# Performance work log

Measured on AMD Instinct MI355X. Metric: run time of the kernel, lower is better.

The kernel has to match this reference:

```python
import jax, jax.numpy as jnp
from jax import lax
import numpy as np

SMOOTH = 1e-4
BN_EPS = 1e-5


def setup_inputs() -> dict:
    key = jax.random.key(0)
    k0, k1, k2, k3 = jax.random.split(key, 4)
    B, C, H, W = 8, 256, 32, 32
    heads, head_dim = 8, 64
    inner = heads * head_dim
    x = jax.random.normal(k0, (B, C, H, W), jnp.float32)
    w_qkv = jax.random.normal(k1, (3 * inner, C, 3, 3), jnp.float32) * 0.02
    head_scale = jax.random.normal(k2, (heads,), jnp.float32)
    w_out = jax.random.normal(k3, (C, inner, 1, 1), jnp.float32) * 0.05
    gamma = jnp.ones((C,), jnp.float32)
    beta = jnp.zeros((C,), jnp.float32)
    return {"x": x, "w_qkv": w_qkv, "head_scale": head_scale,
            "w_out": w_out, "gamma": gamma, "beta": beta}


def _relative_pos_dis(H, W):
    yy, xx = jnp.meshgrid(jnp.arange(H), jnp.arange(W), indexing="ij")
    y = yy.reshape(-1).astype(jnp.float32)
    x = xx.reshape(-1).astype(jnp.float32)
    dy = (y[:, None] - y[None, :]) / H
    dx = (x[:, None] - x[None, :]) / W
    return dy * dy + dx * dx  # [HW, HW]


def reference(x, w_qkv, head_scale, w_out, gamma, beta):
    B, C, H, W = x.shape
    heads = head_scale.shape[0]
    N = H * W
    # qkv 3x3 conv, no bias
    qkv = lax.conv_general_dilated(x, w_qkv, (1, 1), "SAME",
                                   dimension_numbers=("NCHW", "OIHW", "NCHW"))
    inner = qkv.shape[1] // 3
    d = inner // heads
    q, k, v = jnp.split(qkv, 3, axis=1)
    # 'b (g d) h w -> b g (h w) d'
    def resh(t):
        return t.reshape(B, heads, d, N).transpose(0, 1, 3, 2)
    q, k, v = resh(q), resh(k), resh(v)
    # cosine-similarity attention (smoothed)
    attn = jnp.einsum("bgnd,bgmd->bgnm", q, k)
    qn = jnp.sqrt(jnp.sum(q * q, axis=-1) + SMOOTH)  # [B,g,N]
    kn = jnp.sqrt(jnp.sum(k * k, axis=-1) + SMOOTH)
    attn = attn / (qn[:, :, :, None] * kn[:, :, None, :] + SMOOTH)
    # learned per-head Gaussian positional bias
    s = jax.nn.sigmoid(head_scale) * (0.4 - 0.003) + 0.003
    scale_factor = 1.0 / (2.0 * s * s)  # [g]
    dis = _relative_pos_dis(H, W)  # [N,N]
    pb = jnp.exp(-scale_factor[:, None, None] * dis[None, :, :])
    pb = pb / jnp.sum(pb, axis=-1, keepdims=True)
    attn = attn * pb[None]
    out = jnp.einsum("bgnm,bgmd->bgnd", attn, v)
    # 'b g (h w) d -> b (g d) h w'
    out = out.transpose(0, 1, 3, 2).reshape(B, inner, H, W)
    # output projection: 1x1 conv + BatchNorm2d (train-mode batch stats) + ReLU
    out = lax.conv_general_dilated(out, w_out, (1, 1), "VALID",
                                   dimension_numbers=("NCHW", "OIHW", "NCHW"))
    mean = jnp.mean(out, axis=(0, 2, 3))
    var = jnp.mean((out - mean[None, :, None, None]) ** 2, axis=(0, 2, 3))
    out = (out - mean[None, :, None, None]) * (
        gamma[None, :, None, None] * lax.rsqrt(var + BN_EPS)[None, :, None, None]
    ) + beta[None, :, None, None]
    return jax.nn.relu(out)
```

## Files before the change

kernel.cpp:

```cpp
#include <hip/hip_runtime.h>
#include <math.h>

#define SMOOTH 1e-4f
#define BN_EPS 1e-5f

constexpr int Bn = 8;
constexpr int Cc = 256;
constexpr int Nn = 1024;
constexpr int G = 8;
constexpr int INNER = 512;
constexpr int OC = 1536;
constexpr int KK = 2304;

typedef unsigned short u16;
typedef __bf16 bf16x8 __attribute__((ext_vector_type(8)));
typedef float f32x4 __attribute__((ext_vector_type(4)));
typedef unsigned short us8 __attribute__((ext_vector_type(8)));
typedef unsigned short us4 __attribute__((ext_vector_type(4)));

__device__ __forceinline__ u16 f2bf(float f) {
  unsigned int u = __float_as_uint(f);
  unsigned int r = (u + 0x7fffu + ((u >> 16) & 1u)) >> 16;
  return (u16)r;
}
__device__ __forceinline__ float bf2f(u16 u) {
  return __uint_as_float(((unsigned int)u) << 16);
}

__device__ __forceinline__ float waveSum(float v) {
#pragma unroll
  for (int off = 32; off > 0; off >>= 1) v += __shfl_xor(v, off, 64);
  return v;
}

__device__ __forceinline__ void gl16(const u16* g, u16* l) {
  __builtin_amdgcn_global_load_lds(
      (const __attribute__((address_space(1))) unsigned int*)g,
      (__attribute__((address_space(3))) unsigned int*)l, 16, 0, 0);
}

__device__ __forceinline__ bf16x8 ld8(const u16* p) {
  return __builtin_bit_cast(bf16x8, *reinterpret_cast<const us8*>(p));
}

__device__ __forceinline__ void barrier_raw() {
  asm volatile("" ::: "memory");
  __builtin_amdgcn_s_barrier();
  asm volatile("" ::: "memory");
  __builtin_amdgcn_sched_barrier(0);
}

__device__ __forceinline__ bf16x8 ldfrag(const u16* base, int row, int col) {
  int idx = (row * 64 + col) ^ ((row & 7) << 3);
  return ld8(base + idx);
}

__global__ __launch_bounds__(256) void prep_kernel(
    const float* __restrict__ wq, const float* __restrict__ wout,
    const float* __restrict__ x, const float* __restrict__ head_scale,
    u16* __restrict__ wA, u16* __restrict__ wB, u16* __restrict__ B2,
    float* __restrict__ etab, float* __restrict__ idn) {
  __shared__ __align__(16) char smraw[13824];
  const int bid = blockIdx.x;
  const int tid = threadIdx.x;

  if (bid < 1536) {
    float* sw = (float*)smraw;
    const int oc = bid;
    for (int i = tid; i < KK; i += 256) sw[i] = wq[(size_t)oc * KK + i];
    __syncthreads();
#pragma unroll
    for (int j = 0; j < 2; ++j) {
      int c8 = tid + j * 256;
      if (c8 < KK / 8) {
        us8 v;
#pragma unroll
        for (int e = 0; e < 8; ++e) {
          int k = c8 * 8 + e;
          int tap = k >> 8, ic = k & 255;
          v[e] = f2bf(sw[ic * 9 + tap]);
        }
        *reinterpret_cast<us8*>(wA + (size_t)oc * KK + c8 * 8) = v;
      }
    }
  } else if (bid < 1600) {
    const int idx = (bid - 1536) * 256 + tid;
    const float4 a = reinterpret_cast<const float4*>(wout)[idx * 2];
    const float4 b = reinterpret_cast<const float4*>(wout)[idx * 2 + 1];
    us8 v;
    v[0] = f2bf(a.x); v[1] = f2bf(a.y); v[2] = f2bf(a.z); v[3] = f2bf(a.w);
    v[4] = f2bf(b.x); v[5] = f2bf(b.y); v[6] = f2bf(b.z); v[7] = f2bf(b.w);
    reinterpret_cast<us8*>(wB)[idx] = v;
  } else if (bid < 2624) {
    u16* sxt = (u16*)smraw;
    const int lb = bid - 1600;
    const int b = lb >> 7;
    const int y = (lb >> 2) & 31;
    const int icc = lb & 3;
    const int ic0 = icc * 64;
    const float* xb = x + (size_t)b * Cc * Nn;
    {
      const int px = tid & 31;
      const int ic_off = tid >> 5;
#pragma unroll
      for (int r = 0; r < 3; ++r) {
        const int row = y - 1 + r;
        const bool rv = (row >= 0) && (row < 32);
#pragma unroll
        for (int pass = 0; pass < 8; ++pass) {
          const int ic2 = pass * 8 + ic_off;
          float v = rv ? xb[(size_t)(ic0 + ic2) * Nn + row * 32 + px] : 0.f;
          sxt[(r * 32 + px) * 72 + ic2] = f2bf(v);
        }
      }
    }
    __syncthreads();
    const int c8 = tid & 7;
    const int opx = tid >> 3;
    u16* dst = B2 + ((size_t)b * 1024 + y * 32 + opx) * KK + ic0 + c8 * 8;
    const us8 zero = {0, 0, 0, 0, 0, 0, 0, 0};
#pragma unroll
    for (int tap = 0; tap < 9; ++tap) {
      const int dy = tap / 3 - 1, dx = tap % 3 - 1;
      const int sxx = opx + dx;
      const bool cv = (sxx >= 0) && (sxx < 32);
      const int spos = (dy + 1) * 32 + sxx;
      us8 val = cv ? *reinterpret_cast<const us8*>(sxt + spos * 72 + c8 * 8) : zero;
      *reinterpret_cast<us8*>(dst + tap * 256) = val;
    }
  } else {
    float* et = (float*)smraw;
    float* rsum = (float*)smraw + 64;
    const int g = bid - 2624;
    const float hs = head_scale[g];
    const float sg = 1.f / (1.f + __expf(-hs));
    const float s = sg * (0.4f - 0.003f) + 0.003f;
    const float sf = 1.f / (2.f * s * s);
    if (tid < 64) {
      float v = 0.f;
      if (tid < 63) {
        float d = (float)(tid - 31) * (1.f / 32.f);
        v = __expf(-sf * d * d);
      }
      et[tid] = v;
      etab[g * 64 + tid] = v;
    }
    __syncthreads();
    if (tid < 32) {
      float sum = 0.f;
#pragma unroll
      for (int ym = 0; ym < 32; ++ym) sum += et[tid - ym + 31];
      rsum[tid] = sum;
    }
    __syncthreads();
    for (int i = tid; i < 1024; i += 256)
      idn[g * 1024 + i] = 1.f / (rsum[i >> 5] * rsum[i & 31]);
  }
}

__global__ __launch_bounds__(512, 1) void qkv_gemm_kernel(
    const u16* __restrict__ wA, const u16* __restrict__ B2,
    const float* __restrict__ idn,
    u16* __restrict__ qt, u16* __restrict__ ktp, u16* __restrict__ vt) {
  const int tid = threadIdx.x;
  const int lane = tid & 63;
  const int wv = tid >> 6;
  const int wm = wv >> 2, wn = wv & 3;
  const int h = lane >> 4, l15 = lane & 15;
  const int wgid = ((int)blockIdx.x & 7) * 32 + ((int)blockIdx.x >> 3);
  const int bm = wgid & 7;
  const int bn = wgid >> 3;
  const int m0 = bm * 192, n0 = bn * 256;

  __shared__ __align__(16) u16 smem[57344];

  const int arow = tid >> 3;
  const int aslot = (tid & 7) ^ (arow & 7);
  const u16* gA0 = wA + (size_t)(m0 + arow) * KK + aslot * 8;
  const int brow = tid >> 2;
  const int bslot = (tid & 3) ^ (((tid >> 2) & 3) ^ ((tid >> 4) & 3));
  const u16* gB0 = B2 + (size_t)(n0 + brow) * KK + bslot * 8;

  const int aX = l15 & 7;
  const int bX = (l15 & 3) ^ ((l15 >> 2) & 3);
  const u16* aBase = smem + (wm * 96 + l15) * 64;
  const u16* bBase = smem + 12288 + (wn * 64 + l15) * 32;
  const int slA0 = (h ^ aX) * 8;
  const int slA1 = ((4 + h) ^ aX) * 8;
  const int slB = (h ^ bX) * 8;

  f32x4 acc[6][4];
#pragma unroll
  for (int i = 0; i < 6; ++i)
#pragma unroll
    for (int j = 0; j < 4; ++j) acc[i][j] = (f32x4){0.f, 0.f, 0.f, 0.f};

  auto STAGE_A = [&](int pass, int dbuf, int kti) {
    gl16(gA0 + (size_t)pass * 64 * KK + kti * 64,
         smem + dbuf + pass * 4096 + tid * 8);
  };
  auto STAGE_B = [&](int kap, int pass, int dbuf, int kti) {
    gl16(gB0 + (size_t)pass * 128 * KK + kti * 64 + kap * 32,
         smem + dbuf + 12288 + kap * 8192 + pass * 4096 + tid * 8);
  };

  STAGE_A(0, 0, 0); STAGE_A(1, 0, 0); STAGE_A(2, 0, 0);
  STAGE_B(0, 0, 0, 0); STAGE_B(0, 1, 0, 0);
  STAGE_B(1, 0, 0, 0); STAGE_B(1, 1, 0, 0);
  asm volatile("s_waitcnt vmcnt(2)" ::: "memory");
  barrier_raw();

  bf16x8 af[3], bf[4];
#pragma unroll 1
  for (int kt = 0; kt < 36; ++kt) {
    const int buf = (kt & 1) * 28672;
    const int nbuf = 28672 - buf;
    const bool more = (kt < 35);

#pragma unroll
    for (int ni = 0; ni < 4; ++ni) bf[ni] = ld8(bBase + buf + ni * 512 + slB);
#pragma unroll
    for (int q = 0; q < 3; ++q) af[q] = ld8(aBase + buf + q * 1024 + slA0);
    if (more) { STAGE_A(0, nbuf, kt + 1); STAGE_A(1, nbuf, kt + 1); }
    barrier_raw();
    __builtin_amdgcn_s_setprio(1);
#pragma unroll
    for (int q = 0; q < 3; ++q)
#pragma unroll
      for (int ni = 0; ni < 4; ++ni)
        acc[q][ni] = __builtin_amdgcn_mfma_f32_16x16x32_bf16(af[q], bf[ni], acc[q][ni], 0, 0, 0);
    __builtin_amdgcn_s_setprio(0);

#pragma unroll
    for (int q = 0; q < 3; ++q) af[q] = ld8(aBase + buf + (3 + q) * 1024 + slA0);
    if (more) {
      STAGE_A(2, nbuf, kt + 1); STAGE_B(0, 0, nbuf, kt + 1);
      asm volatile("s_waitcnt vmcnt(4)" ::: "memory");
    } else {
      asm volatile("s_waitcnt vmcnt(0)" ::: "memory");
    }
    barrier_raw();
    __builtin_amdgcn_s_setprio(1);
#pragma unroll
    for (int q = 0; q < 3; ++q)
#pragma unroll
      for (int ni = 0; ni < 4; ++ni)
        acc[3 + q][ni] = __builtin_amdgcn_mfma_f32_16x16x32_bf16(af[q], bf[ni], acc[3 + q][ni], 0, 0, 0);
    __builtin_amdgcn_s_setprio(0);

#pragma unroll
    for (int ni = 0; ni < 4; ++ni) bf[ni] = ld8(bBase + buf + 8192 + ni * 512 + slB);
#pragma unroll
    for (int q = 0; q < 3; ++q) af[q] = ld8(aBase + buf + q * 1024 + slA1);
    if (more) { STAGE_B(0, 1, nbuf, kt + 1); STAGE_B(1, 0, nbuf, kt + 1); }
    barrier_raw();
    __builtin_amdgcn_s_setprio(1);
#pragma unroll
    for (int q = 0; q < 3; ++q)
#pragma unroll
      for (int ni = 0; ni < 4; ++ni)
        acc[q][ni] = __builtin_amdgcn_mfma_f32_16x16x32_bf16(af[q], bf[ni], acc[q][ni], 0, 0, 0);
    __builtin_amdgcn_s_setprio(0);

#pragma unroll
    for (int q = 0; q < 3; ++q) af[q] = ld8(aBase + buf + (3 + q) * 1024 + slA1);
    if (more) {
      STAGE_B(1, 1, nbuf, kt + 1);
      asm volatile("s_waitcnt vmcnt(2)" ::: "memory");
    }
    barrier_raw();
    __builtin_amdgcn_s_setprio(1);
#pragma unroll
    for (int q = 0; q < 3; ++q)
#pragma unroll
      for (int ni = 0; ni < 4; ++ni)
        acc[3 + q][ni] = __builtin_amdgcn_mfma_f32_16x16x32_bf16(af[q], bf[ni], acc[3 + q][ni], 0, 0, 0);
    __builtin_amdgcn_s_setprio(0);
  }

  const int b = bn >> 2;
  const int nimgBase = (bn & 3) * 256 + wn * 64;
  float ssF[4], ssH[4];
#pragma unroll
  for (int ni = 0; ni < 4; ++ni) {
    float sF = 0.f, sH = 0.f;
#pragma unroll
    for (int m4 = 0; m4 < 6; ++m4) {
      float s = 0.f;
#pragma unroll
      for (int r = 0; r < 4; ++r) s += acc[m4][ni][r] * acc[m4][ni][r];
      const bool isFull = (wm == 0) ? (m4 < 4) : (m4 >= 2);
      if (isFull) sF += s; else sH += s;
    }
    sF += __shfl_xor(sF, 16, 64); sF += __shfl_xor(sF, 32, 64);
    sH += __shfl_xor(sH, 16, 64); sH += __shfl_xor(sH, 32, 64);
    ssF[ni] = sF; ssH[ni] = sH;
  }
  float* xch = (float*)smem;
  if (h == 0) {
#pragma unroll
    for (int ni = 0; ni < 4; ++ni)
      xch[((wm * 4 + wn) * 4 + ni) * 16 + l15] = ssH[ni];
  }
  __syncthreads();
#pragma unroll
  for (int ni = 0; ni < 4; ++ni)
    ssH[ni] += xch[(((1 - wm) * 4 + wn) * 4 + ni) * 16 + l15];

  const int headF = (wm == 0) ? 3 * bm : 3 * bm + 2;
  const int headH = 3 * bm + 1;
  const int secF = headF >> 3, gF = headF & 7;
  const int secH = headH >> 3, gH = headH & 7;
  float rsF[4], rsH[4];
#pragma unroll
  for (int ni = 0; ni < 4; ++ni) {
    const int nimg = nimgBase + ni * 16 + l15;
    float rf = rsqrtf(ssF[ni] + SMOOTH);
    if (secF == 0) rf *= idn[gF * 1024 + nimg];
    rsF[ni] = rf;
    float rh = rsqrtf(ssH[ni] + SMOOTH);
    if (secH == 0) rh *= idn[gH * 1024 + nimg];
    rsH[ni] = rh;
  }
#pragma unroll
  for (int m4 = 0; m4 < 6; ++m4) {
    const bool isFull = (wm == 0) ? (m4 < 4) : (m4 >= 2);
    const int head = isFull ? headF : headH;
    const int sec = head >> 3, g = head & 7;
    const int d0 = isFull ? ((wm == 0) ? m4 * 16 : (m4 - 2) * 16)
                          : ((wm == 0) ? (m4 - 4) * 16 : 32 + m4 * 16);
    const size_t bg = (size_t)b * G + g;
    if (sec < 2) {
      u16* basep = (sec ? ktp : qt) + bg * 65536;
#pragma unroll
      for (int ni = 0; ni < 4; ++ni) {
        const float rs = isFull ? rsF[ni] : rsH[ni];
        const int nimg = nimgBase + ni * 16 + l15;
        us4 v;
        v[0] = f2bf(acc[m4][ni][0] * rs);
        v[1] = f2bf(acc[m4][ni][1] * rs);
        v[2] = f2bf(acc[m4][ni][2] * rs);
        v[3] = f2bf(acc[m4][ni][3] * rs);
        *reinterpret_cast<us4*>(basep + (size_t)nimg * 64 + d0 + 4 * h) = v;
      }
    } else {
      u16* basep = vt + bg * 65536;
#pragma unroll
      for (int ni = 0; ni < 4; ++ni) {
        const int nimg = nimgBase + ni * 16 + l15;
#pragma unroll
        for (int r = 0; r < 4; ++r)
          basep[(size_t)(d0 + 4 * h + r) * 1024 + nimg] = f2bf(acc[m4][ni][r]);
      }
    }
  }
}

__global__ __launch_bounds__(256, 2) void attn_mfma_kernel(
    const u16* __restrict__ qt, const u16* __restrict__ ktp,
    const u16* __restrict__ vt, const float* __restrict__ etab,
    u16* __restrict__ aout) {
  const int tid = threadIdx.x;
  const int lane = tid & 63;
  const int wv = tid >> 6;
  const int h = lane >> 4;
  const int l15 = lane & 15;
  const int wgid = (blockIdx.x & 7) * 64 + (blockIdx.x >> 3);
  const int g = wgid >> 6;
  const int b = (wgid >> 3) & 7;
  const int nb = wgid & 7;

  __shared__ __align__(16) u16 smem[32768];
  __shared__ float etabL[64];
  u16* sQ = smem;
  u16* sP = smem + 24576 + wv * 2048;

  const size_t bg = (size_t)b * G + g;
  const u16* qg = qt + bg * 65536;
  const u16* kg = ktp + bg * 65536;
  const u16* vg = vt + bg * 65536;

  if (tid < 64) etabL[tid] = etab[g * 64 + tid];

  const int srow = tid >> 3;
  const int scol = ((tid & 7) ^ (srow & 7)) * 8;

#pragma unroll
  for (int pass = 0; pass < 4; ++pass)
    gl16(qg + (size_t)(nb * 128 + pass * 32 + srow) * 64 + scol,
         sQ + pass * 2048 + tid * 8);
#pragma unroll
  for (int pass = 0; pass < 2; ++pass) {
    gl16(kg + (size_t)(pass * 32 + srow) * 64 + scol,
         smem + 8192 + pass * 2048 + tid * 8);
    gl16(vg + (size_t)(pass * 32 + srow) * 1024 + scol,
         smem + 16384 + pass * 2048 + tid * 8);
  }
  __syncthreads();

  float exv[2][4][2];
  int ynr[2][4];
#pragma unroll
  for (int ti = 0; ti < 2; ++ti)
#pragma unroll
    for (int r = 0; r < 4; ++r) {
      int n = nb * 128 + wv * 32 + ti * 16 + 4 * h + r;
      int xn = n & 31;
      ynr[ti][r] = n >> 5;
      exv[ti][r][0] = etabL[xn - l15 + 31];
      exv[ti][r][1] = etabL[xn - l15 + 15];
    }

  f32x4 oacc[2][4];
#pragma unroll
  for (int ti = 0; ti < 2; ++ti)
#pragma unroll
    for (int dj = 0; dj < 4; ++dj) oacc[ti][dj] = (f32x4){0.f, 0.f, 0.f, 0.f};

  const int col8 = h * 8;

  for (int mt = 0; mt < 16; ++mt) {
    const u16* sKb = smem + 8192 + (mt & 1) * 4096;
    const u16* sVb = smem + 16384 + (mt & 1) * 4096;
    if (mt < 15) {
      const int nt2 = mt + 1;
      const int d = nt2 & 1;
#pragma unroll
      for (int pass = 0; pass < 2; ++pass) {
        gl16(kg + (size_t)(nt2 * 64 + pass * 32 + srow) * 64 + scol,
             smem + 8192 + d * 4096 + pass * 2048 + tid * 8);
        gl16(vg + (size_t)(pass * 32 + srow) * 1024 + nt2 * 64 + scol,
             smem + 16384 + d * 4096 + pass * 2048 + tid * 8);
      }
    }

    float eyv[2][4][2];
#pragma unroll
    for (int ti = 0; ti < 2; ++ti)
#pragma unroll
      for (int r = 0; r < 4; ++r) {
        eyv[ti][r][0] = etabL[ynr[ti][r] - 2 * mt + 31];
        eyv[ti][r][1] = etabL[ynr[ti][r] - 2 * mt + 30];
      }

    f32x4 sacc[2][4];
#pragma unroll
    for (int ti = 0; ti < 2; ++ti)
#pragma unroll
      for (int tj = 0; tj < 4; ++tj) sacc[ti][tj] = (f32x4){0.f, 0.f, 0.f, 0.f};
#pragma unroll
    for (int kk = 0; kk < 2; ++kk) {
      bf16x8 aq0 = ldfrag(sQ, wv * 32 + l15, kk * 32 + col8);
      bf16x8 aq1 = ldfrag(sQ, wv * 32 + 16 + l15, kk * 32 + col8);
#pragma unroll
      for (int tj = 0; tj < 4; ++tj) {
        bf16x8 bk = ldfrag(sKb, tj * 16 + l15, kk * 32 + col8);
        sacc[0][tj] = __builtin_amdgcn_mfma_f32_16x16x32_bf16(aq0, bk, sacc[0][tj], 0, 0, 0);
        sacc[1][tj] = __builtin_amdgcn_mfma_f32_16x16x32_bf16(aq1, bk, sacc[1][tj], 0, 0, 0);
      }
    }

#pragma unroll
    for (int tj = 0; tj < 4; ++tj) {
#pragma unroll
      for (int ti = 0; ti < 2; ++ti) {
#pragma unroll
        for (int r = 0; r < 4; ++r) {
          float wgt = sacc[ti][tj][r] * (eyv[ti][r][tj >> 1] * exv[ti][r][tj & 1]);
          int nl = ti * 16 + 4 * h + r;
          int pidx = (nl * 64 + tj * 16 + l15) ^ ((nl & 7) << 3);
          sP[pidx] = f2bf(wgt);
        }
      }
    }

#pragma unroll
    for (int km = 0; km < 2; ++km) {
      bf16x8 ap0 = ldfrag(sP, l15, km * 32 + col8);
      bf16x8 ap1 = ldfrag(sP, 16 + l15, km * 32 + col8);
#pragma unroll
      for (int dj = 0; dj < 4; ++dj) {
        bf16x8 bvv = ldfrag(sVb, dj * 16 + l15, km * 32 + col8);
        oacc[0][dj] = __builtin_amdgcn_mfma_f32_16x16x32_bf16(ap0, bvv, oacc[0][dj], 0, 0, 0);
        oacc[1][dj] = __builtin_amdgcn_mfma_f32_16x16x32_bf16(ap1, bvv, oacc[1][dj], 0, 0, 0);
      }
    }
    __syncthreads();
  }

  u16* sO = smem + 8192;
#pragma unroll
  for (int ti = 0; ti < 2; ++ti)
#pragma unroll
    for (int dj = 0; dj < 4; ++dj)
#pragma unroll
      for (int r = 0; r < 4; ++r) {
        int nl = wv * 32 + ti * 16 + 4 * h + r;
        int idx = (nl * 64 + dj * 16 + l15) ^ ((nl & 7) << 3);
        sO[idx] = f2bf(oacc[ti][dj][r]);
      }
  __syncthreads();
  {
    const int row = tid >> 1, c = (tid & 1) * 4;
    us8* dst = reinterpret_cast<us8*>(aout + (bg * 1024 + (size_t)nb * 128 + row) * 64);
#pragma unroll
    for (int k = 0; k < 4; ++k) {
      int idx = (row * 64 + (c + k) * 8) ^ ((row & 7) << 3);
      dst[c + k] = *reinterpret_cast<const us8*>(sO + idx);
    }
  }
}

__global__ __launch_bounds__(256, 4) void conv1x1_mfma_kernel(
    const u16* __restrict__ aout, const u16* __restrict__ wB,
    u16* __restrict__ proj) {
  const int tid = threadIdx.x;
  const int lane = tid & 63;
  const int wv = tid >> 6;
  const int wr = wv >> 1, wc = wv & 1;
  const int h = lane >> 4, l15 = lane & 15;
  const int bm = blockIdx.x & 3;
  const int ntile = blockIdx.x >> 2;
  const int b = ntile >> 4;
  const int n0 = (ntile & 15) * 64;
  const int c0 = bm * 64;

  __shared__ __align__(16) u16 smem[16384];

  f32x4 acc[2][2];
#pragma unroll
  for (int i = 0; i < 2; ++i)
#pragma unroll
    for (int j = 0; j < 2; ++j) acc[i][j] = (f32x4){0.f, 0.f, 0.f, 0.f};

  const int srow = tid >> 3;
  const int scol = (tid & 7) * 8;

  auto STG = [&](int ks) {
    const int d = ks & 1;
#pragma unroll
    for (int pass = 0; pass < 2; ++pass) {
      gl16(wB + (size_t)(c0 + pass * 32 + srow) * 512 + ks * 64 + scol,
           smem + d * 4096 + pass * 2048 + tid * 8);
      gl16(aout + ((size_t)(b * G + ks) * 1024 + n0 + pass * 32 + srow) * 64 + scol,
           smem + 8192 + d * 4096 + pass * 2048 + tid * 8);
    }
  };

  STG(0);
  __syncthreads();
  for (int ks = 0; ks < 8; ++ks) {
    if (ks < 7) STG(ks + 1);
    const u16* sA = smem + (ks & 1) * 4096;
    const u16* sB = smem + 8192 + (ks & 1) * 4096;
#pragma unroll
    for (int kk = 0; kk < 2; ++kk) {
      bf16x8 af[2], bv[2];
#pragma unroll
      for (int mt = 0; mt < 2; ++mt)
        af[mt] = ld8(sA + (wr * 32 + mt * 16 + l15) * 64 + kk * 32 + h * 8);
#pragma unroll
      for (int nt = 0; nt < 2; ++nt)
        bv[nt] = ld8(sB + (wc * 32 + nt * 16 + l15) * 64 + kk * 32 + h * 8);
#pragma unroll
      for (int mt = 0; mt < 2; ++mt)
#pragma unroll
        for (int nt = 0; nt < 2; ++nt)
          acc[mt][nt] = __builtin_amdgcn_mfma_f32_16x16x32_bf16(af[mt], bv[nt], acc[mt][nt], 0, 0, 0);
    }
    __syncthreads();
  }

#pragma unroll
  for (int mt = 0; mt < 2; ++mt)
#pragma unroll
    for (int nt = 0; nt < 2; ++nt)
#pragma unroll
      for (int r = 0; r < 4; ++r) {
        const int c = c0 + wr * 32 + mt * 16 + 4 * h + r;
        const int n = n0 + wc * 32 + nt * 16 + l15;
        proj[((size_t)b * Cc + c) * Nn + n] = f2bf(acc[mt][nt][r]);
      }
}

__global__ __launch_bounds__(256) void bn_stats_kernel(
    const u16* __restrict__ proj, float* __restrict__ stats) {
  const int c = blockIdx.x;
  const int tid = threadIdx.x;
  float s = 0.f, s2 = 0.f;
  for (int b = 0; b < Bn; ++b) {
    us4 v = reinterpret_cast<const us4*>(proj + ((size_t)b * Cc + c) * Nn)[tid];
#pragma unroll
    for (int j = 0; j < 4; ++j) {
      float f = bf2f(v[j]);
      s += f;
      s2 += f * f;
    }
  }
  s = waveSum(s);
  s2 = waveSum(s2);
  __shared__ float r1[4], r2[4];
  if ((tid & 63) == 0) { r1[tid >> 6] = s; r2[tid >> 6] = s2; }
  __syncthreads();
  if (tid == 0) {
    float S = r1[0] + r1[1] + r1[2] + r1[3];
    float S2 = r2[0] + r2[1] + r2[2] + r2[3];
    const float invM = 1.f / (float)(Bn * Nn);
    float mean = S * invM;
    float var = S2 * invM - mean * mean;
    stats[c] = mean;
    stats[Cc + c] = rsqrtf(var + BN_EPS);
  }
}

__global__ __launch_bounds__(256) void bn_apply_kernel(
    const u16* __restrict__ proj, const float* __restrict__ stats,
    const float* __restrict__ gamma, const float* __restrict__ beta,
    float* __restrict__ out) {
  const int idx = blockIdx.x * 256 + threadIdx.x;
  const int flat = idx << 2;
  const int c = (flat >> 10) & (Cc - 1);
  us4 v = reinterpret_cast<const us4*>(proj)[idx];
  const float mean = stats[c];
  const float sc = stats[Cc + c] * gamma[c];
  const float sh = beta[c];
  float4 o;
  o.x = fmaxf((bf2f(v[0]) - mean) * sc + sh, 0.f);
  o.y = fmaxf((bf2f(v[1]) - mean) * sc + sh, 0.f);
  o.z = fmaxf((bf2f(v[2]) - mean) * sc + sh, 0.f);
  o.w = fmaxf((bf2f(v[3]) - mean) * sc + sh, 0.f);
  reinterpret_cast<float4*>(out)[idx] = o;
}

extern "C" void kernel_launch(void* const* d_in, const int* in_sizes, int n_in,
                              void* d_out, int out_size, void* d_ws, size_t ws_size,
                              hipStream_t stream) {
  const float* x = (const float*)d_in[0];
  const float* w_qkv = (const float*)d_in[1];
  const float* head_scale = (const float*)d_in[2];
  const float* w_out = (const float*)d_in[3];
  const float* gamma = (const float*)d_in[4];
  const float* beta = (const float*)d_in[5];
  float* out = (float*)d_out;

  char* w = (char*)d_ws;
  u16* qt = (u16*)(w + 0);
  u16* kt = (u16*)(w + 8388608);
  u16* vt = (u16*)(w + 16777216);
  u16* wA = (u16*)(w + 25165824);
  u16* aout = (u16*)(w + 25165824);
  u16* B2 = (u16*)(w + 33554432);
  u16* proj = (u16*)(w + 33554432);
  float* etab = (float*)(w + 71303168);
  float* idn = (float*)(w + 71305216);
  float* stats = (float*)(w + 71860224);
  u16* wB = (u16*)(w + 71862272);

  prep_kernel<<<dim3(2632), dim3(256), 0, stream>>>(
      w_qkv, w_out, x, head_scale, wA, wB, B2, etab, idn);
  qkv_gemm_kernel<<<dim3(256), dim3(512), 0, stream>>>(wA, B2, idn, qt, kt, vt);
  attn_mfma_kernel<<<dim3(512), dim3(256), 0, stream>>>(qt, kt, vt, etab, aout);
  conv1x1_mfma_kernel<<<dim3(512), dim3(256), 0, stream>>>(aout, wB, proj);
  bn_stats_kernel<<<dim3(Cc), dim3(256), 0, stream>>>(proj, stats);
  bn_apply_kernel<<<dim3((Bn * Cc * Nn / 4) / 256), dim3(256), 0, stream>>>(proj, stats, gamma, beta, out);
}
```

Baseline: 122.3 us.

## Replace materialized im2col buffer with implicit im2col loads in QKV GEMM

The prep kernel no longer writes a full 9-tap im2col matrix (8192x2304 bf16). It now writes only a channel-last bf16 transpose of x. The QKV GEMM computes the shifted source pixel for each tap on the fly and points out-of-bounds rows at a small zero page. This removes the large im2col write and its re-read traffic. In exchange it adds per-load address arithmetic and less contiguous global reads in the GEMM's B staging.

```diff
diff --git a/kernel.cpp b/kernel.cpp
--- a/kernel.cpp
+++ b/kernel.cpp
@@ -58,9 +58,10 @@
 __global__ __launch_bounds__(256) void prep_kernel(
     const float* __restrict__ wq, const float* __restrict__ wout,
     const float* __restrict__ x, const float* __restrict__ head_scale,
-    u16* __restrict__ wA, u16* __restrict__ wB, u16* __restrict__ B2,
-    float* __restrict__ etab, float* __restrict__ idn) {
-  __shared__ __align__(16) char smraw[13824];
+    u16* __restrict__ wA, u16* __restrict__ wB, u16* __restrict__ xT,
+    u16* __restrict__ zpage, float* __restrict__ etab,
+    float* __restrict__ idn) {
+  __shared__ __align__(16) char smraw[9216];
   const int bid = blockIdx.x;
   const int tid = threadIdx.x;
 
@@ -91,47 +92,37 @@
     v[0] = f2bf(a.x); v[1] = f2bf(a.y); v[2] = f2bf(a.z); v[3] = f2bf(a.w);
     v[4] = f2bf(b.x); v[5] = f2bf(b.y); v[6] = f2bf(b.z); v[7] = f2bf(b.w);
     reinterpret_cast<us8*>(wB)[idx] = v;
-  } else if (bid < 2624) {
+    if (bid == 1536 && tid < 128) zpage[tid] = 0;
+  } else if (bid < 2112) {
     u16* sxt = (u16*)smraw;
     const int lb = bid - 1600;
-    const int b = lb >> 7;
-    const int y = (lb >> 2) & 31;
-    const int icc = lb & 3;
-    const int ic0 = icc * 64;
+    const int b = lb >> 6;
+    const int nt = (lb >> 1) & 31;
+    const int icc = lb & 1;
+    const int n0 = nt * 32;
+    const int ic0 = icc * 128;
     const float* xb = x + (size_t)b * Cc * Nn;
     {
       const int px = tid & 31;
-      const int ic_off = tid >> 5;
-#pragma unroll
-      for (int r = 0; r < 3; ++r) {
-        const int row = y - 1 + r;
-        const bool rv = (row >= 0) && (row < 32);
-#pragma unroll
-        for (int pass = 0; pass < 8; ++pass) {
-          const int ic2 = pass * 8 + ic_off;
-          float v = rv ? xb[(size_t)(ic0 + ic2) * Nn + row * 32 + px] : 0.f;
-          sxt[(r * 32 + px) * 72 + ic2] = f2bf(v);
-        }
+      const int ic8 = tid >> 5;
+#pragma unroll
+      for (int i2 = 0; i2 < 16; ++i2) {
+        const int ic = ic8 * 16 + i2;
+        sxt[px * 136 + ic] = f2bf(xb[(size_t)(ic0 + ic) * Nn + n0 + px]);
       }
     }
     __syncthreads();
     const int c8 = tid & 7;
-    const int opx = tid >> 3;
-    u16* dst = B2 + ((size_t)b * 1024 + y * 32 + opx) * KK + ic0 + c8 * 8;
-    const us8 zero = {0, 0, 0, 0, 0, 0, 0, 0};
-#pragma unroll
-    for (int tap = 0; tap < 9; ++tap) {
-      const int dy = tap / 3 - 1, dx = tap % 3 - 1;
-      const int sxx = opx + dx;
-      const bool cv = (sxx >= 0) && (sxx < 32);
-      const int spos = (dy + 1) * 32 + sxx;
-      us8 val = cv ? *reinterpret_cast<const us8*>(sxt + spos * 72 + c8 * 8) : zero;
-      *reinterpret_cast<us8*>(dst + tap * 256) = val;
-    }
+    const int px = tid >> 3;
+    u16* dst = xT + (((size_t)b * 1024 + n0 + px) * 256) + ic0 + c8 * 8;
+#pragma unroll
+    for (int c32 = 0; c32 < 2; ++c32)
+      *reinterpret_cast<us8*>(dst + c32 * 64) =
+          *reinterpret_cast<const us8*>(sxt + px * 136 + c32 * 64 + c8 * 8);
   } else {
     float* et = (float*)smraw;
     float* rsum = (float*)smraw + 64;
-    const int g = bid - 2624;
+    const int g = bid - 2112;
     const float hs = head_scale[g];
     const float sg = 1.f / (1.f + __expf(-hs));
     const float s = sg * (0.4f - 0.003f) + 0.003f;
@@ -159,8 +150,8 @@
 }
 
 __global__ __launch_bounds__(512, 1) void qkv_gemm_kernel(
-    const u16* __restrict__ wA, const u16* __restrict__ B2,
-    const float* __restrict__ idn,
+    const u16* __restrict__ wA, const u16* __restrict__ xT,
+    const u16* __restrict__ zpage, const float* __restrict__ idn,
     u16* __restrict__ qt, u16* __restrict__ ktp, u16* __restrict__ vt) {
   const int tid = threadIdx.x;
   const int lane = tid & 63;
@@ -170,16 +161,16 @@
   const int wgid = ((int)blockIdx.x & 7) * 32 + ((int)blockIdx.x >> 3);
   const int bm = wgid & 7;
   const int bn = wgid >> 3;
-  const int m0 = bm * 192, n0 = bn * 256;
+  const int m0 = bm * 192;
 
   __shared__ __align__(16) u16 smem[57344];
 
   const int arow = tid >> 3;
   const int aslot = (tid & 7) ^ (arow & 7);
   const u16* gA0 = wA + (size_t)(m0 + arow) * KK + aslot * 8;
-  const int brow = tid >> 2;
-  const int bslot = (tid & 3) ^ (((tid >> 2) & 3) ^ ((tid >> 4) & 3));
-  const u16* gB0 = B2 + (size_t)(n0 + brow) * KK + bslot * 8;
+  const int bslot8 = ((tid & 3) ^ (((tid >> 2) & 3) ^ ((tid >> 4) & 3))) * 8;
+  const int pimgBase = ((bn & 3) << 8) + (tid >> 2);
+  const u16* xTb = xT + (size_t)(bn >> 2) * (1024 * 256);
 
   const int aX = l15 & 7;
   const int bX = (l15 & 3) ^ ((l15 >> 2) & 3);
@@ -200,8 +191,20 @@
          smem + dbuf + pass * 4096 + tid * 8);
   };
   auto STAGE_B = [&](int kap, int pass, int dbuf, int kti) {
-    gl16(gB0 + (size_t)pass * 128 * KK + kti * 64 + kap * 32,
-         smem + dbuf + 12288 + kap * 8192 + pass * 4096 + tid * 8);
+    const int tap = kti >> 2;
+    const int dyq = (tap * 11) >> 5;
+    const int ddx = tap - 3 * dyq - 1;
+    const int ddy = dyq - 1;
+    const int pimg = pimgBase + pass * 128;
+    const int sx = (pimg & 31) + ddx;
+    const int sy = (pimg >> 5) + ddy;
+    const u16* src;
+    if (((unsigned)sx < 32u) && ((unsigned)sy < 32u))
+      src = xTb + ((size_t)(pimg + ddx + ddy * 32) * 256 +
+                   ((kti & 3) << 6) + kap * 32 + bslot8);
+    else
+      src = zpage;
+    gl16(src, smem + dbuf + 12288 + kap * 8192 + pass * 4096 + tid * 8);
   };
 
   STAGE_A(0, 0, 0); STAGE_A(1, 0, 0); STAGE_A(2, 0, 0);
@@ -649,16 +652,17 @@
   u16* vt = (u16*)(w + 16777216);
   u16* wA = (u16*)(w + 25165824);
   u16* aout = (u16*)(w + 25165824);
-  u16* B2 = (u16*)(w + 33554432);
-  u16* proj = (u16*)(w + 33554432);
+  u16* xT = (u16*)(w + 33554432);
+  u16* proj = (u16*)(w + 37748736);
   float* etab = (float*)(w + 71303168);
   float* idn = (float*)(w + 71305216);
+  u16* zpage = (u16*)(w + 71337984);
   float* stats = (float*)(w + 71860224);
   u16* wB = (u16*)(w + 71862272);
 
-  prep_kernel<<<dim3(2632), dim3(256), 0, stream>>>(
-      w_qkv, w_out, x, head_scale, wA, wB, B2, etab, idn);
-  qkv_gemm_kernel<<<dim3(256), dim3(512), 0, stream>>>(wA, B2, idn, qt, kt, vt);
+  prep_kernel<<<dim3(2120), dim3(256), 0, stream>>>(
+      w_qkv, w_out, x, head_scale, wA, wB, xT, zpage, etab, idn);
+  qkv_gemm_kernel<<<dim3(256), dim3(512), 0, stream>>>(wA, xT, zpage, idn, qt, kt, vt);
   attn_mfma_kernel<<<dim3(512), dim3(256), 0, stream>>>(qt, kt, vt, etab, aout);
   conv1x1_mfma_kernel<<<dim3(512), dim3(256), 0, stream>>>(aout, wB, proj);
   bn_stats_kernel<<<dim3(Cc), dim3(256), 0, stream>>>(proj, stats);
```

Measured after the change: 118.5 us. -3.1%, faster.
